# Performance work log

Hardware: AMD Instinct MI355X
Metric: run time of the kernel (lower is better)

The kernel has to match this reference:

```python
import jax, jax.numpy as jnp
import numpy as np
import math

HEAD = 16
D_MODEL = 1024
HEAD_DIM = D_MODEL // HEAD
B, S = 2, 2048


def setup_inputs() -> dict:
    key = jax.random.key(0)
    ks = jax.random.split(key, 9)
    sc = 1.0 / math.sqrt(D_MODEL)
    return {
        "q": jax.random.normal(ks[0], (B, S, D_MODEL), dtype=jnp.float32),
        "k": jax.random.normal(ks[1], (B, S, D_MODEL), dtype=jnp.float32),
        "v": jax.random.normal(ks[2], (B, S, D_MODEL), dtype=jnp.float32),
        "mask": jax.random.randint(ks[3], (B, 1, S, S), 0, 2, dtype=jnp.int32),
        "wq": jax.random.normal(ks[4], (D_MODEL, D_MODEL), dtype=jnp.float32) * sc,
        "wk": jax.random.normal(ks[5], (D_MODEL, D_MODEL), dtype=jnp.float32) * sc,
        "wv": jax.random.normal(ks[6], (D_MODEL, D_MODEL), dtype=jnp.float32) * sc,
        "wo": jax.random.normal(ks[7], (D_MODEL, D_MODEL), dtype=jnp.float32) * sc,
        "bo": jax.random.normal(ks[8], (D_MODEL,), dtype=jnp.float32) * 0.01,
    }


def reference(q, k, v, mask, wq, wk, wv, wo, bo):
    N, Lq, _ = q.shape
    Lk = k.shape[1]
    # projections (bias-free linears)
    qh = (q @ wq).reshape(N, Lq, HEAD, HEAD_DIM)
    kh = (k @ wk).reshape(N, Lk, HEAD, HEAD_DIM)
    vh = (v @ wv).reshape(N, Lk, HEAD, HEAD_DIM)
    # full [N, H, Lq, Lk] score matrix, as in original
    scores = jnp.einsum('nqha,nkha->nhqk', qh, kh)
    scores = jnp.where(mask == 0, jnp.float32(-1e10), scores)
    attn = jax.nn.softmax(scores / math.sqrt(HEAD_DIM), axis=-1)
    out = jnp.einsum('nhqk,nkha->nqha', attn, vh).reshape(N, Lq, D_MODEL)
    return out @ wo + bo
```

## Files before the change

kernel.cpp:

```cpp
#include <hip/hip_runtime.h>

typedef unsigned short ushort_t;
typedef __attribute__((ext_vector_type(8))) __bf16 bf16x8;
typedef __attribute__((ext_vector_type(4))) float f32x4;
typedef __attribute__((ext_vector_type(4))) unsigned int u32x4;
typedef __attribute__((ext_vector_type(4))) unsigned short u16x4;

#define NB 2
#define SS 2048
#define NH 16
#define DH 64
#define DM 1024
#define MM 4096

#define QK_SCALE 0.1803368801111204f

__device__ __forceinline__ ushort_t f2bf(float f){
  unsigned u = __builtin_bit_cast(unsigned, f);
  unsigned r = u + 0x7FFFu + ((u >> 16) & 1u);
  return (ushort_t)(r >> 16);
}

__device__ __forceinline__ void load_lds16(const void* g, void* l){
  __builtin_amdgcn_global_load_lds(
      (const __attribute__((address_space(1))) unsigned int*)g,
      (__attribute__((address_space(3))) unsigned int*)l, 16, 0, 0);
}

__global__ __launch_bounds__(256) void cvt3(const float* __restrict__ q,
                                            const float* __restrict__ k,
                                            const float* __restrict__ v,
                                            ushort_t* qo, ushort_t* ko, ushort_t* vo, int n){
  int z = blockIdx.z;
  const float* src = (z == 0) ? q : (z == 1) ? k : v;
  ushort_t* dst    = (z == 0) ? qo : (z == 1) ? ko : vo;
  int i = (blockIdx.x * blockDim.x + threadIdx.x) * 4;
  if (i < n){
    f32x4 w = *(const f32x4*)(src + i);
    u16x4 o = { f2bf(w[0]), f2bf(w[1]), f2bf(w[2]), f2bf(w[3]) };
    *(u16x4*)(dst + i) = o;
  }
}

__global__ __launch_bounds__(256) void wtrans4(const float* __restrict__ W0, const float* __restrict__ W1,
                                               const float* __restrict__ W2, const float* __restrict__ W3,
                                               ushort_t* T0, ushort_t* T1, ushort_t* T2, ushort_t* T3){
  __shared__ float t[32][33];
  int z = blockIdx.z;
  const float* W = (z == 0) ? W0 : (z == 1) ? W1 : (z == 2) ? W2 : W3;
  ushort_t* Wt   = (z == 0) ? T0 : (z == 1) ? T1 : (z == 2) ? T2 : T3;
  int k0 = blockIdx.x * 32, n0 = blockIdx.y * 32;
  int tx = threadIdx.x, ty = threadIdx.y;
  #pragma unroll
  for (int i = 0; i < 4; i++)
    t[ty + 8*i][tx] = W[(size_t)(k0 + ty + 8*i) * DM + (n0 + tx)];
  __syncthreads();
  #pragma unroll
  for (int i = 0; i < 4; i++)
    Wt[(size_t)(n0 + ty + 8*i) * DM + (k0 + tx)] = f2bf(t[tx][ty + 8*i]);
}

__global__ __launch_bounds__(256) void mask_expand(const int* __restrict__ mask,
                                                   ushort_t* __restrict__ mexp){
  int id = blockIdx.x * 4 + (threadIdx.x >> 6);
  int lane = threadIdx.x & 63;
  int t = id & 31; int qgrp = (id >> 5) & 127; int b = id >> 12;
  int lc = lane & 15, g = lane >> 4;

  const int* mrow = mask + (((size_t)b * SS) + qgrp * 16) * SS + t * 64 + lane;
  unsigned long long mybits = 0;
  #pragma unroll
  for (int r = 0; r < 16; r++){
    unsigned long long bits = __ballot(mrow[(size_t)r * SS] != 0);
    if (lc == r) mybits = bits;
  }

  unsigned w8[8];
  #pragma unroll
  for (int w = 0; w < 8; w++){
    int c = w >> 2, i = w & 3;
    int kv0 = (2*c + (i >> 1))*16 + 4*g + 2*(i & 1);
    w8[w] = (((mybits >> kv0) & 1ULL) ? 0xFFFFu : 0u)
          | (((mybits >> (kv0 + 1)) & 1ULL) ? 0xFFFF0000u : 0u);
  }
  ushort_t* dst = mexp + ((size_t)id) * 1024 + lane * 16;
  u32x4 a = { w8[0], w8[1], w8[2], w8[3] };
  u32x4 bb = { w8[4], w8[5], w8[6], w8[7] };
  *(u32x4*)dst = a;
  *(u32x4*)(dst + 8) = bb;
}

__global__ __launch_bounds__(256) void vtrans(const ushort_t* __restrict__ vh,
                                              ushort_t* __restrict__ vt){
  __shared__ ushort_t t[64][65];
  int bh = blockIdx.y, s0 = blockIdx.x * 64;
  int tid = threadIdx.x;
  const ushort_t* src = vh + (size_t)bh * SS * DH + (size_t)s0 * DH;
  #pragma unroll
  for (int i = 0; i < 2; i++){
    int id = tid + 256*i; int r = id >> 3, c = id & 7;
    union { u32x4 v; ushort_t s[8]; } u;
    u.v = *(const u32x4*)(src + r*64 + c*8);
    #pragma unroll
    for (int j = 0; j < 8; j++) t[r][c*8 + j] = u.s[j];
  }
  __syncthreads();
  ushort_t* dst = vt + (size_t)bh * DH * SS;
  #pragma unroll
  for (int i = 0; i < 2; i++){
    int id = tid + 256*i; int d = id >> 3, c8 = id & 7;
    union { u32x4 v; ushort_t s[8]; } u;
    #pragma unroll
    for (int j = 0; j < 8; j++){
      int p = c8*8 + j;
      int srck = ((p >> 5) << 5) + (((p & 7) >> 2) << 4) + (((p >> 3) & 3) << 2) + (p & 3);
      u.s[j] = t[srck][d];
    }
    *(u32x4*)(dst + (size_t)d * SS + s0 + c8*8) = u.v;
  }
}

__global__ __launch_bounds__(256) void gemm_qkv(
    const ushort_t* A0, const ushort_t* A1, const ushort_t* A2,
    const ushort_t* B0, const ushort_t* B1, const ushort_t* B2,
    ushort_t* C0, ushort_t* C1, ushort_t* C2){
  __shared__ __align__(16) char smem[32768];
  char* As = smem; char* Bs = smem + 16384;

  int flat = blockIdx.x + 32 * blockIdx.y + 256 * blockIdx.z;
  int nswz = (flat & 7) * 96 + (flat >> 3);
  int z = nswz >> 8; int rem = nswz & 255;
  int m0 = (rem & 31) * 128, n0 = (rem >> 5) * 128;

  const ushort_t* A  = (z == 0) ? A0 : (z == 1) ? A1 : A2;
  const ushort_t* Bt = (z == 0) ? B0 : (z == 1) ? B1 : B2;
  ushort_t* Cb       = (z == 0) ? C0 : (z == 1) ? C1 : C2;

  int tid = threadIdx.x, wid = tid >> 6, lane = tid & 63;
  int lc = lane & 15, g = lane >> 4;
  int wm = wid >> 1, wn = wid & 1;

  f32x4 acc[4][4] = {};
  for (int kt = 0; kt < DM / 64; kt++){
    __syncthreads();
    int k0 = kt * 64;
    #pragma unroll
    for (int i = 0; i < 4; i++){
      int id = tid + 256*i; int r = id >> 3, c = id & 7;
      load_lds16(A  + (size_t)(m0 + r) * DM + k0 + ((c ^ (r & 7)) << 3), As + id*16);
      load_lds16(Bt + (size_t)(n0 + r) * DM + k0 + ((c ^ (r & 7)) << 3), Bs + id*16);
    }
    __syncthreads();
    #pragma unroll
    for (int f = 0; f < 2; f++){
      bf16x8 af[4], bfr[4];
      #pragma unroll
      for (int i = 0; i < 4; i++){
        int ar = wm*64 + i*16 + lc;
        af[i] = *(const bf16x8*)(As + ar*128 + (((f*4 + g) ^ (ar & 7)) << 4));
        int br = wn*64 + i*16 + lc;
        bfr[i] = *(const bf16x8*)(Bs + br*128 + (((f*4 + g) ^ (br & 7)) << 4));
      }
      #pragma unroll
      for (int mi = 0; mi < 4; mi++)
        #pragma unroll
        for (int ni = 0; ni < 4; ni++)
          acc[mi][ni] = __builtin_amdgcn_mfma_f32_16x16x32_bf16(af[mi], bfr[ni], acc[mi][ni], 0, 0, 0);
    }
  }
  float oscale = (z == 0) ? QK_SCALE : 1.0f;
  #pragma unroll
  for (int mi = 0; mi < 4; mi++)
    #pragma unroll
    for (int ni = 0; ni < 4; ni++)
      #pragma unroll
      for (int reg = 0; reg < 4; reg++){
        int m = m0 + wm*64 + mi*16 + g*4 + reg;
        int n = n0 + wn*64 + ni*16 + lc;
        int b = m >> 11, s = m & (SS - 1), h = n >> 6, d = n & 63;
        Cb[(((size_t)(b*NH + h)) * SS + s) * DH + d] = f2bf(acc[mi][ni][reg] * oscale);
      }
}

__global__ __launch_bounds__(256) void gemm_wo(const ushort_t* __restrict__ A,
                                               const ushort_t* __restrict__ Bt,
                                               float* __restrict__ Cf,
                                               const float* __restrict__ bias){
  __shared__ __align__(16) char smem[24576];
  char* As = smem; char* Bs = smem + 16384;

  int flat = blockIdx.x + 32 * blockIdx.y;
  int nswz = (flat & 7) * 64 + (flat >> 3);
  int m0 = (nswz & 31) * 128, n0 = (nswz >> 5) * 64;

  int tid = threadIdx.x, wid = tid >> 6, lane = tid & 63;
  int lc = lane & 15, g = lane >> 4;
  int wm = wid >> 1, wn = wid & 1;

  f32x4 acc[4][2] = {};
  for (int kt = 0; kt < DM / 64; kt++){
    __syncthreads();
    int k0 = kt * 64;
    #pragma unroll
    for (int i = 0; i < 4; i++){
      int id = tid + 256*i; int r = id >> 3, c = id & 7;
      load_lds16(A + (size_t)(m0 + r) * DM + k0 + ((c ^ (r & 7)) << 3), As + id*16);
    }
    #pragma unroll
    for (int i = 0; i < 2; i++){
      int id = tid + 256*i; int r = id >> 3, c = id & 7;
      load_lds16(Bt + (size_t)(n0 + r) * DM + k0 + ((c ^ (r & 7)) << 3), Bs + id*16);
    }
    __syncthreads();
    #pragma unroll
    for (int f = 0; f < 2; f++){
      bf16x8 af[4], bfr[2];
      #pragma unroll
      for (int i = 0; i < 4; i++){
        int ar = wm*64 + i*16 + lc;
        af[i] = *(const bf16x8*)(As + ar*128 + (((f*4 + g) ^ (ar & 7)) << 4));
      }
      #pragma unroll
      for (int i = 0; i < 2; i++){
        int br = wn*32 + i*16 + lc;
        bfr[i] = *(const bf16x8*)(Bs + br*128 + (((f*4 + g) ^ (br & 7)) << 4));
      }
      #pragma unroll
      for (int mi = 0; mi < 4; mi++)
        #pragma unroll
        for (int ni = 0; ni < 2; ni++)
          acc[mi][ni] = __builtin_amdgcn_mfma_f32_16x16x32_bf16(af[mi], bfr[ni], acc[mi][ni], 0, 0, 0);
    }
  }
  #pragma unroll
  for (int mi = 0; mi < 4; mi++)
    #pragma unroll
    for (int ni = 0; ni < 2; ni++)
      #pragma unroll
      for (int reg = 0; reg < 4; reg++){
        int m = m0 + wm*64 + mi*16 + g*4 + reg;
        int n = n0 + wn*32 + ni*16 + lc;
        Cf[(size_t)m * DM + n] = acc[mi][ni][reg] + bias[n];
      }
}

__global__ __launch_bounds__(512, 4) void attn_fwd(
    const ushort_t* __restrict__ qh, const ushort_t* __restrict__ kh,
    const ushort_t* __restrict__ vt, const ushort_t* __restrict__ mexp,
    ushort_t* __restrict__ ao){
  __shared__ __align__(16) char smem[32768];

  int L = blockIdx.x;
  int xcd = L & 7, slot = L >> 3;
  int bh = xcd * 4 + (slot >> 4);
  int q0 = (slot & 15) * 128;
  int b = bh >> 4;

  int tid = threadIdx.x, wid = tid >> 6, lane = tid & 63;
  int lc = lane & 15, g = lane >> 4;

  const size_t hoff = (size_t)bh * SS * DH;
  const ushort_t* Qb = qh + hoff;
  const ushort_t* Kb = kh + hoff;
  const ushort_t* Vb = vt + hoff;

  int qrow = q0 + wid*16 + lc;
  bf16x8 qf[2];
  #pragma unroll
  for (int c = 0; c < 2; c++)
    qf[c] = *(const bf16x8*)(Qb + (size_t)qrow * DH + c*32 + 8*g);

  const ushort_t* mbase = mexp + (((size_t)b * 128 + (q0 >> 4) + wid) * 32) * 1024 + lane * 16;

  int sw0 = ((0*4 + g) ^ (lc & 7)) << 4;
  int sw1 = ((1*4 + g) ^ (lc & 7)) << 4;

  bf16x8 onesf;
  { union { bf16x8 v; unsigned w[4]; } u;
    unsigned x = (lc == 0) ? 0x3F803F80u : 0u;
    u.w[0] = x; u.w[1] = x; u.w[2] = x; u.w[3] = x; onesf = u.v; }

  f32x4 o[4] = {};
  f32x4 o4 = {};

  auto stage = [&](int bufsel, int it){
    int kv0 = it * 64;
    char* dst = smem + bufsel * 16384;
    #pragma unroll
    for (int i = 0; i < 2; i++){
      int id = tid + 512*i;
      int tl = id >> 9; int r = (id >> 3) & 63; int c = id & 7;
      const ushort_t* src = tl
        ? Vb + (size_t)r * SS + kv0 + ((c ^ (r & 7)) << 3)
        : Kb + (size_t)(kv0 + r) * DH + ((c ^ (r & 7)) << 3);
      load_lds16(src, dst + id*16);
    }
  };

  u32x4 mwa = *(const u32x4*)(mbase);
  u32x4 mwb = *(const u32x4*)(mbase + 8);
  stage(0, 0);
  __syncthreads();

  for (int it = 0; it < 32; it++){
    int cur = it & 1;
    if (it < 31) stage(cur ^ 1, it + 1);

    int itn = (it < 31) ? it + 1 : 31;
    u32x4 mna = *(const u32x4*)(mbase + (size_t)itn * 1024);
    u32x4 mnb = *(const u32x4*)(mbase + (size_t)itn * 1024 + 8);

    const char* Ks = smem + cur*16384;
    const char* Vs = Ks + 8192;

    f32x4 sc4[4];
    #pragma unroll
    for (int nt = 0; nt < 4; nt++){
      f32x4 a = {};
      const char* krow = Ks + (nt*16 + lc) * 128;
      bf16x8 kf0 = *(const bf16x8*)(krow + sw0);
      bf16x8 kf1 = *(const bf16x8*)(krow + sw1);
      a = __builtin_amdgcn_mfma_f32_16x16x32_bf16(kf0, qf[0], a, 0, 0, 0);
      a = __builtin_amdgcn_mfma_f32_16x16x32_bf16(kf1, qf[1], a, 0, 0, 0);
      sc4[nt] = a;
    }

    bf16x8 pa[2];
    #pragma unroll
    for (int c = 0; c < 2; c++){
      union { bf16x8 v; unsigned w[4]; } up;
      #pragma unroll
      for (int i = 0; i < 4; i++){
        int j0 = 2*i, j1 = 2*i + 1;
        float e0 = __builtin_amdgcn_exp2f(sc4[c*2 + (j0 >> 2)][j0 & 3]);
        float e1 = __builtin_amdgcn_exp2f(sc4[c*2 + (j1 >> 2)][j1 & 3]);
        unsigned lo = __builtin_bit_cast(unsigned, e0) + 0x8000u;
        unsigned hi = __builtin_bit_cast(unsigned, e1) + 0x8000u;
        up.w[i] = __builtin_amdgcn_perm(hi, lo, 0x07060302u) & (c ? mwb[i] : mwa[i]);
      }
      pa[c] = up.v;
    }

    #pragma unroll
    for (int c = 0; c < 2; c++){
      int off = c ? sw1 : sw0;
      #pragma unroll
      for (int dt = 0; dt < 4; dt++){
        bf16x8 vf = *(const bf16x8*)(Vs + (dt*16 + lc) * 128 + off);
        o[dt] = __builtin_amdgcn_mfma_f32_16x16x32_bf16(pa[c], vf, o[dt], 0, 0, 0);
      }
      o4 = __builtin_amdgcn_mfma_f32_16x16x32_bf16(pa[c], onesf, o4, 0, 0, 0);
    }

    __syncthreads();
    mwa = mna; mwb = mnb;
  }

  #pragma unroll
  for (int reg = 0; reg < 4; reg++){
    float l = __shfl(o4[reg], lane & 48);
    float inv = 1.0f / l;
    int srow = q0 + wid*16 + g*4 + reg;
    size_t base = ((size_t)b * SS + srow) * DM + (size_t)(bh & 15) * DH;
    #pragma unroll
    for (int dt = 0; dt < 4; dt++)
      ao[base + dt*16 + lc] = f2bf(o[dt][reg] * inv);
  }
}

extern "C" void kernel_launch(void* const* d_in, const int* in_sizes, int n_in,
                              void* d_out, int out_size, void* d_ws, size_t ws_size,
                              hipStream_t stream){
  const float* q    = (const float*)d_in[0];
  const float* k    = (const float*)d_in[1];
  const float* v    = (const float*)d_in[2];
  const int*   mask = (const int*)d_in[3];
  const float* wq   = (const float*)d_in[4];
  const float* wk   = (const float*)d_in[5];
  const float* wv   = (const float*)d_in[6];
  const float* wo   = (const float*)d_in[7];
  const float* bo   = (const float*)d_in[8];
  float* out = (float*)d_out;

  char* ws = (char*)d_ws;
  ushort_t* qb  = (ushort_t*)(ws + 0x0000000);
  ushort_t* kb  = (ushort_t*)(ws + 0x0800000);
  ushort_t* vb  = (ushort_t*)(ws + 0x1000000);
  ushort_t* wt0 = (ushort_t*)(ws + 0x1800000);
  ushort_t* wt1 = (ushort_t*)(ws + 0x1A00000);
  ushort_t* wt2 = (ushort_t*)(ws + 0x1C00000);
  ushort_t* wt3 = (ushort_t*)(ws + 0x1E00000);
  ushort_t* mexp = (ushort_t*)(ws + 0x2000000);
  ushort_t* qhB = (ushort_t*)(ws + 0x3000000);
  ushort_t* khB = (ushort_t*)(ws + 0x3800000);
  ushort_t* vhB = (ushort_t*)(ws + 0x4000000);
  ushort_t* vtB = (ushort_t*)(ws + 0x0000000);
  ushort_t* aoB = (ushort_t*)(ws + 0x4000000);

  const int nElem = MM * DM;
  cvt3<<<dim3(nElem/1024, 1, 3), 256, 0, stream>>>(q, k, v, qb, kb, vb, nElem);

  wtrans4<<<dim3(32, 32, 4), dim3(32, 8), 0, stream>>>(wq, wk, wv, wo, wt0, wt1, wt2, wt3);

  mask_expand<<<NB * 128 * 32 / 4, 256, 0, stream>>>(mask, mexp);

  gemm_qkv<<<dim3(32, 8, 3), 256, 0, stream>>>(
      qb, kb, vb, wt0, wt1, wt2, qhB, khB, vhB);

  vtrans<<<dim3(SS/64, NB*NH), 256, 0, stream>>>(vhB, vtB);

  attn_fwd<<<512, 512, 0, stream>>>(qhB, khB, vtB, mexp, aoB);

  gemm_wo<<<dim3(32, 16), 256, 0, stream>>>(aoB, wt3, out, bo);
}
```

Measured before the change: 262.8 us.

## Fuse prep kernels, compute V transpose in QKV GEMM, add MFMA priority hints

Merges the input conversion, weight transpose and mask expansion kernels into one prep launch. Removes the separate V transpose kernel by computing V^T directly in gemm_qkv with swapped operands and a permuted store. Reorders gemm_wo tile mapping and raises wave priority around MFMA blocks in attention. Trades fewer launches and one less memory pass for strided epilogue stores.

Result: faster. 244.7 us (-6.9%).

```diff
diff --git a/kernel.cpp b/kernel.cpp
--- a/kernel.cpp
+++ b/kernel.cpp
@@ -27,54 +27,53 @@
       (__attribute__((address_space(3))) unsigned int*)l, 16, 0, 0);
 }
 
-__global__ __launch_bounds__(256) void cvt3(const float* __restrict__ q,
-                                            const float* __restrict__ k,
-                                            const float* __restrict__ v,
-                                            ushort_t* qo, ushort_t* ko, ushort_t* vo, int n){
-  int z = blockIdx.z;
-  const float* src = (z == 0) ? q : (z == 1) ? k : v;
-  ushort_t* dst    = (z == 0) ? qo : (z == 1) ? ko : vo;
-  int i = (blockIdx.x * blockDim.x + threadIdx.x) * 4;
-  if (i < n){
+__global__ __launch_bounds__(256) void prep(
+    const float* __restrict__ q, const float* __restrict__ k, const float* __restrict__ v,
+    ushort_t* qo, ushort_t* ko, ushort_t* vo,
+    const float* __restrict__ W0, const float* __restrict__ W1,
+    const float* __restrict__ W2, const float* __restrict__ W3,
+    ushort_t* T0, ushort_t* T1, ushort_t* T2, ushort_t* T3,
+    const int* __restrict__ mask, ushort_t* __restrict__ mexp){
+  __shared__ float t[32][33];
+  int y = blockIdx.y, bx = blockIdx.x, tid = threadIdx.x;
+
+  if (y < 3){
+    const float* src = (y == 0) ? q : (y == 1) ? k : v;
+    ushort_t* dst    = (y == 0) ? qo : (y == 1) ? ko : vo;
+    int i = (bx * 256 + tid) * 4;
     f32x4 w = *(const f32x4*)(src + i);
     u16x4 o = { f2bf(w[0]), f2bf(w[1]), f2bf(w[2]), f2bf(w[3]) };
     *(u16x4*)(dst + i) = o;
-  }
-}
-
-__global__ __launch_bounds__(256) void wtrans4(const float* __restrict__ W0, const float* __restrict__ W1,
-                                               const float* __restrict__ W2, const float* __restrict__ W3,
-                                               ushort_t* T0, ushort_t* T1, ushort_t* T2, ushort_t* T3){
-  __shared__ float t[32][33];
-  int z = blockIdx.z;
-  const float* W = (z == 0) ? W0 : (z == 1) ? W1 : (z == 2) ? W2 : W3;
-  ushort_t* Wt   = (z == 0) ? T0 : (z == 1) ? T1 : (z == 2) ? T2 : T3;
-  int k0 = blockIdx.x * 32, n0 = blockIdx.y * 32;
-  int tx = threadIdx.x, ty = threadIdx.y;
-  #pragma unroll
-  for (int i = 0; i < 4; i++)
-    t[ty + 8*i][tx] = W[(size_t)(k0 + ty + 8*i) * DM + (n0 + tx)];
-  __syncthreads();
-  #pragma unroll
-  for (int i = 0; i < 4; i++)
-    Wt[(size_t)(n0 + ty + 8*i) * DM + (k0 + tx)] = f2bf(t[tx][ty + 8*i]);
-}
-
-__global__ __launch_bounds__(256) void mask_expand(const int* __restrict__ mask,
-                                                   ushort_t* __restrict__ mexp){
-  int id = blockIdx.x * 4 + (threadIdx.x >> 6);
-  int lane = threadIdx.x & 63;
-  int t = id & 31; int qgrp = (id >> 5) & 127; int b = id >> 12;
+    return;
+  }
+  if (y == 3){
+    int z = bx >> 10;
+    const float* W = (z == 0) ? W0 : (z == 1) ? W1 : (z == 2) ? W2 : W3;
+    ushort_t* Wt   = (z == 0) ? T0 : (z == 1) ? T1 : (z == 2) ? T2 : T3;
+    int k0 = ((bx >> 5) & 31) * 32, n0 = (bx & 31) * 32;
+    int tx = tid & 31, ty = tid >> 5;
+    #pragma unroll
+    for (int i = 0; i < 4; i++)
+      t[ty + 8*i][tx] = W[(size_t)(k0 + ty + 8*i) * DM + (n0 + tx)];
+    __syncthreads();
+    #pragma unroll
+    for (int i = 0; i < 4; i++)
+      Wt[(size_t)(n0 + ty + 8*i) * DM + (k0 + tx)] = f2bf(t[tx][ty + 8*i]);
+    return;
+  }
+  if (bx >= 2048) return;
+  int id = bx * 4 + (tid >> 6);
+  int lane = tid & 63;
+  int tt = id & 31; int qgrp = (id >> 5) & 127; int b = id >> 12;
   int lc = lane & 15, g = lane >> 4;
 
-  const int* mrow = mask + (((size_t)b * SS) + qgrp * 16) * SS + t * 64 + lane;
+  const int* mrow = mask + (((size_t)b * SS) + qgrp * 16) * SS + tt * 64 + lane;
   unsigned long long mybits = 0;
   #pragma unroll
   for (int r = 0; r < 16; r++){
     unsigned long long bits = __ballot(mrow[(size_t)r * SS] != 0);
     if (lc == r) mybits = bits;
   }
-
   unsigned w8[8];
   #pragma unroll
   for (int w = 0; w < 8; w++){
@@ -90,51 +89,21 @@
   *(u32x4*)(dst + 8) = bb;
 }
 
-__global__ __launch_bounds__(256) void vtrans(const ushort_t* __restrict__ vh,
-                                              ushort_t* __restrict__ vt){
-  __shared__ ushort_t t[64][65];
-  int bh = blockIdx.y, s0 = blockIdx.x * 64;
-  int tid = threadIdx.x;
-  const ushort_t* src = vh + (size_t)bh * SS * DH + (size_t)s0 * DH;
-  #pragma unroll
-  for (int i = 0; i < 2; i++){
-    int id = tid + 256*i; int r = id >> 3, c = id & 7;
-    union { u32x4 v; ushort_t s[8]; } u;
-    u.v = *(const u32x4*)(src + r*64 + c*8);
-    #pragma unroll
-    for (int j = 0; j < 8; j++) t[r][c*8 + j] = u.s[j];
-  }
-  __syncthreads();
-  ushort_t* dst = vt + (size_t)bh * DH * SS;
-  #pragma unroll
-  for (int i = 0; i < 2; i++){
-    int id = tid + 256*i; int d = id >> 3, c8 = id & 7;
-    union { u32x4 v; ushort_t s[8]; } u;
-    #pragma unroll
-    for (int j = 0; j < 8; j++){
-      int p = c8*8 + j;
-      int srck = ((p >> 5) << 5) + (((p & 7) >> 2) << 4) + (((p >> 3) & 3) << 2) + (p & 3);
-      u.s[j] = t[srck][d];
-    }
-    *(u32x4*)(dst + (size_t)d * SS + s0 + c8*8) = u.v;
-  }
-}
-
 __global__ __launch_bounds__(256) void gemm_qkv(
     const ushort_t* A0, const ushort_t* A1, const ushort_t* A2,
     const ushort_t* B0, const ushort_t* B1, const ushort_t* B2,
-    ushort_t* C0, ushort_t* C1, ushort_t* C2){
+    ushort_t* C0, ushort_t* C1, ushort_t* vtOut){
   __shared__ __align__(16) char smem[32768];
-  char* As = smem; char* Bs = smem + 16384;
+  char* Xs = smem; char* Ys = smem + 16384;
 
   int flat = blockIdx.x + 32 * blockIdx.y + 256 * blockIdx.z;
   int nswz = (flat & 7) * 96 + (flat >> 3);
   int z = nswz >> 8; int rem = nswz & 255;
-  int m0 = (rem & 31) * 128, n0 = (rem >> 5) * 128;
-
-  const ushort_t* A  = (z == 0) ? A0 : (z == 1) ? A1 : A2;
-  const ushort_t* Bt = (z == 0) ? B0 : (z == 1) ? B1 : B2;
-  ushort_t* Cb       = (z == 0) ? C0 : (z == 1) ? C1 : C2;
+  int x0 = (z == 2) ? (rem & 7) * 128 : (rem >> 3) * 128;
+  int y0 = (z == 2) ? (rem >> 3) * 128 : (rem & 7) * 128;
+
+  const ushort_t* P = (z == 0) ? A0 : (z == 1) ? A1 : B2;
+  const ushort_t* Q = (z == 0) ? B0 : (z == 1) ? B1 : A2;
 
   int tid = threadIdx.x, wid = tid >> 6, lane = tid & 63;
   int lc = lane & 15, g = lane >> 4;
@@ -147,8 +116,8 @@
     #pragma unroll
     for (int i = 0; i < 4; i++){
       int id = tid + 256*i; int r = id >> 3, c = id & 7;
-      load_lds16(A  + (size_t)(m0 + r) * DM + k0 + ((c ^ (r & 7)) << 3), As + id*16);
-      load_lds16(Bt + (size_t)(n0 + r) * DM + k0 + ((c ^ (r & 7)) << 3), Bs + id*16);
+      load_lds16(P + (size_t)(x0 + r) * DM + k0 + ((c ^ (r & 7)) << 3), Xs + id*16);
+      load_lds16(Q + (size_t)(y0 + r) * DM + k0 + ((c ^ (r & 7)) << 3), Ys + id*16);
     }
     __syncthreads();
     #pragma unroll
@@ -157,9 +126,9 @@
       #pragma unroll
       for (int i = 0; i < 4; i++){
         int ar = wm*64 + i*16 + lc;
-        af[i] = *(const bf16x8*)(As + ar*128 + (((f*4 + g) ^ (ar & 7)) << 4));
+        af[i] = *(const bf16x8*)(Xs + ar*128 + (((f*4 + g) ^ (ar & 7)) << 4));
         int br = wn*64 + i*16 + lc;
-        bfr[i] = *(const bf16x8*)(Bs + br*128 + (((f*4 + g) ^ (br & 7)) << 4));
+        bfr[i] = *(const bf16x8*)(Ys + br*128 + (((f*4 + g) ^ (br & 7)) << 4));
       }
       #pragma unroll
       for (int mi = 0; mi < 4; mi++)
@@ -168,18 +137,37 @@
           acc[mi][ni] = __builtin_amdgcn_mfma_f32_16x16x32_bf16(af[mi], bfr[ni], acc[mi][ni], 0, 0, 0);
     }
   }
-  float oscale = (z == 0) ? QK_SCALE : 1.0f;
-  #pragma unroll
-  for (int mi = 0; mi < 4; mi++)
-    #pragma unroll
-    for (int ni = 0; ni < 4; ni++)
-      #pragma unroll
-      for (int reg = 0; reg < 4; reg++){
-        int m = m0 + wm*64 + mi*16 + g*4 + reg;
-        int n = n0 + wn*64 + ni*16 + lc;
-        int b = m >> 11, s = m & (SS - 1), h = n >> 6, d = n & 63;
-        Cb[(((size_t)(b*NH + h)) * SS + s) * DH + d] = f2bf(acc[mi][ni][reg] * oscale);
-      }
+
+  if (z < 2){
+    ushort_t* Cb = (z == 0) ? C0 : C1;
+    float oscale = (z == 0) ? QK_SCALE : 1.0f;
+    #pragma unroll
+    for (int mi = 0; mi < 4; mi++)
+      #pragma unroll
+      for (int ni = 0; ni < 4; ni++)
+        #pragma unroll
+        for (int reg = 0; reg < 4; reg++){
+          int m = x0 + wm*64 + mi*16 + g*4 + reg;
+          int n = y0 + wn*64 + ni*16 + lc;
+          int b = m >> 11, s = m & (SS - 1), h = n >> 6, d = n & 63;
+          Cb[(((size_t)(b*NH + h)) * SS + s) * DH + d] = f2bf(acc[mi][ni][reg] * oscale);
+        }
+  } else {
+    #pragma unroll
+    for (int mi = 0; mi < 4; mi++)
+      #pragma unroll
+      for (int ni = 0; ni < 4; ni++)
+        #pragma unroll
+        for (int reg = 0; reg < 4; reg++){
+          int rr = x0 + wm*64 + mi*16 + g*4 + reg;
+          int cc = y0 + wn*64 + ni*16 + lc;
+          int h = rr >> 6, d = rr & 63;
+          int b = cc >> 11, s = cc & (SS - 1);
+          int s64 = ni*16 + lc;
+          int p = (s64 & 32) | ((s64 & 12) << 1) | ((s64 & 16) >> 2) | (s64 & 3);
+          vtOut[((size_t)(b*NH + h) * DH + d) * SS + (s & ~63) + p] = f2bf(acc[mi][ni][reg]);
+        }
+  }
 }
 
 __global__ __launch_bounds__(256) void gemm_wo(const ushort_t* __restrict__ A,
@@ -191,7 +179,7 @@
 
   int flat = blockIdx.x + 32 * blockIdx.y;
   int nswz = (flat & 7) * 64 + (flat >> 3);
-  int m0 = (nswz & 31) * 128, n0 = (nswz >> 5) * 64;
+  int m0 = (nswz >> 4) * 128, n0 = (nswz & 15) * 64;
 
   int tid = threadIdx.x, wid = tid >> 6, lane = tid & 63;
   int lc = lane & 15, g = lane >> 4;
@@ -314,6 +302,7 @@
     const char* Vs = Ks + 8192;
 
     f32x4 sc4[4];
+    __builtin_amdgcn_s_setprio(1);
     #pragma unroll
     for (int nt = 0; nt < 4; nt++){
       f32x4 a = {};
@@ -324,6 +313,7 @@
       a = __builtin_amdgcn_mfma_f32_16x16x32_bf16(kf1, qf[1], a, 0, 0, 0);
       sc4[nt] = a;
     }
+    __builtin_amdgcn_s_setprio(0);
 
     bf16x8 pa[2];
     #pragma unroll
@@ -341,6 +331,7 @@
       pa[c] = up.v;
     }
 
+    __builtin_amdgcn_s_setprio(1);
     #pragma unroll
     for (int c = 0; c < 2; c++){
       int off = c ? sw1 : sw0;
@@ -351,6 +342,7 @@
       }
       o4 = __builtin_amdgcn_mfma_f32_16x16x32_bf16(pa[c], onesf, o4, 0, 0, 0);
     }
+    __builtin_amdgcn_s_setprio(0);
 
     __syncthreads();
     mwa = mna; mwb = mnb;
@@ -393,21 +385,15 @@
   ushort_t* mexp = (ushort_t*)(ws + 0x2000000);
   ushort_t* qhB = (ushort_t*)(ws + 0x3000000);
   ushort_t* khB = (ushort_t*)(ws + 0x3800000);
-  ushort_t* vhB = (ushort_t*)(ws + 0x4000000);
-  ushort_t* vtB = (ushort_t*)(ws + 0x0000000);
-  ushort_t* aoB = (ushort_t*)(ws + 0x4000000);
-
-  const int nElem = MM * DM;
-  cvt3<<<dim3(nElem/1024, 1, 3), 256, 0, stream>>>(q, k, v, qb, kb, vb, nElem);
-
-  wtrans4<<<dim3(32, 32, 4), dim3(32, 8), 0, stream>>>(wq, wk, wv, wo, wt0, wt1, wt2, wt3);
-
-  mask_expand<<<NB * 128 * 32 / 4, 256, 0, stream>>>(mask, mexp);
+  ushort_t* vtB = (ushort_t*)(ws + 0x4000000);
+  ushort_t* aoB = (ushort_t*)(ws + 0x0800000);
+
+  prep<<<dim3(4096, 5), 256, 0, stream>>>(q, k, v, qb, kb, vb,
+                                          wq, wk, wv, wo, wt0, wt1, wt2, wt3,
+                                          mask, mexp);
 
   gemm_qkv<<<dim3(32, 8, 3), 256, 0, stream>>>(
-      qb, kb, vb, wt0, wt1, wt2, qhB, khB, vhB);
-
-  vtrans<<<dim3(SS/64, NB*NH), 256, 0, stream>>>(vhB, vtB);
+      qb, kb, vb, wt0, wt1, wt2, qhB, khB, vtB);
 
   attn_fwd<<<512, 512, 0, stream>>>(qhB, khB, vtB, mexp, aoB);
 
```
